# Optimization experiments

Measured on AMD Instinct MI355X. Metric: run time of the kernel, lower is better.

The kernel has to match this reference:

```python
import jax, jax.numpy as jnp
import numpy as np

B, LN, LT, D, DIN, H = 8, 64, 256, 1024, 2048, 4
LN_EPS = 1e-5
F16_EPS = float(np.finfo(np.float16).eps)


def setup_inputs() -> dict:
    key = jax.random.key(0)
    ks = jax.random.split(key, 16)
    n = lambda k, sh: jax.random.normal(k, sh, dtype=jnp.float32)
    s = 0.02
    z = lambda sh: jnp.zeros(sh, jnp.float32)
    return {
        "text_embeds": n(ks[0], (B, LT, D)),
        "node_embeds": n(ks[1], (B, LN, D)),
        "Wq": n(ks[2], (D, H * D)) * s, "bq": z((H * D,)),
        "Wk": n(ks[3], (D, H * D)) * s, "bk": z((H * D,)),
        "Wv": n(ks[4], (D, H * D)) * s, "bv": z((H * D,)),
        "Wo": n(ks[5], (H * D, D)) * s, "bo": z((D,)),
        "ln_g": jnp.ones((D,), jnp.float32), "ln_b": z((D,)),
        "aqW": n(ks[6], (D, D)) * s, "aqb": z((D,)),
        "akW": n(ks[7], (D, D)) * s, "akb": z((D,)),
        "att_v": n(ks[8], (D,)) * (1.0 / np.sqrt(D)),
        "att_b": z((D,)),
        "dp1W": n(ks[9], (D, DIN // 2)) * s, "dp1b": z((DIN // 2,)),
        "dp2W": n(ks[10], (DIN // 2, DIN)) * s, "dp2b": z((DIN,)),
        "gnn_mask": jax.random.randint(ks[11], (B, LN), 0, 2),
        "lm_mask": jax.random.randint(ks[12], (B, LT), 0, 2),
    }


def _forward(text_embeds, node_embeds, Wq, bq, Wk, bk, Wv, bv, Wo, bo, ln_g, ln_b,
             aqW, aqb, akW, akb, att_v, att_b, dp1W, dp1b, dp2W, dp2b,
             gnn_mask, lm_mask):
    x = node_embeds  # (B, LN, D)

    # ---- selfAttention_prompt: each of 4 heads has full width D ----
    def heads(w, b):
        return (x @ w + b).reshape(B, LN, H, D).transpose(0, 2, 1, 3)  # (B,H,LN,D)

    Q, K, V = heads(Wq, bq), heads(Wk, bk), heads(Wv, bv)
    A = jnp.einsum('bhqd,bhkd->bhqk', Q, K) / jnp.sqrt(jnp.float32(D))
    A = jnp.where(gnn_mask[:, None, None, :] == 0, -jnp.inf, A)
    alpha = jax.nn.softmax(A, axis=-1)
    out = jnp.einsum('bhqk,bhkd->bhqd', alpha, V)
    out = out.transpose(0, 2, 1, 3).reshape(B, LN, H * D)
    out = out @ Wo + bo + x
    # LayerNorm (torch default eps=1e-5)
    mu = out.mean(-1, keepdims=True)
    var = ((out - mu) ** 2).mean(-1, keepdims=True)
    H2 = (out - mu) / jnp.sqrt(var + LN_EPS) * ln_g + ln_b  # (B, LN, D)

    # ---- AdditiveAttention (Bahdanau): value_proj is unused in the original ----
    q = H2 @ aqW + aqb            # (B, LN, D)
    k = text_embeds @ akW + akb   # (B, LT, D)
    e = jnp.einsum('bqkd,d->bqk',
                   jnp.tanh(q[:, :, None, :] + k[:, None, :, :] + att_b), att_v)
    e = jnp.where(lm_mask[:, None, :] == 0, -jnp.inf, e)
    w = jax.nn.softmax(e, axis=-1)            # (B, LN, LT)
    H3 = jnp.einsum('bqk,bkd->bqd', w, text_embeds)  # context with raw V

    # ---- filter_Pool: masked mean over nodes ----
    m = gnn_mask.astype(H3.dtype)[:, :, None]
    cnt = jnp.clip(m.sum(1), F16_EPS, None)   # (B, 1)
    H4 = (H3 * m).sum(1) / cnt                # (B, D)

    # ---- domain projector (exact GELU like torch) ----
    Z = jax.nn.gelu(H4 @ dp1W + dp1b, approximate=False) @ dp2W + dp2b
    return Z  # (B, DIN)


def reference(text_embeds, node_embeds, Wq, bq, Wk, bk, Wv, bv, Wo, bo, ln_g, ln_b,
              aqW, aqb, akW, akb, att_v, att_b, dp1W, dp1b, dp2W, dp2b,
              gnn_mask, lm_mask):
    return _forward(text_embeds, node_embeds, Wq, bq, Wk, bk, Wv, bv, Wo, bo,
                    ln_g, ln_b, aqW, aqb, akW, akb, att_v, att_b,
                    dp1W, dp1b, dp2W, dp2b, gnn_mask, lm_mask)
```

## Files before the change

### kernel.cpp

```cpp
#include <hip/hip_runtime.h>
#include <hip/hip_bf16.h>
#include <math.h>

#define NB 8
#define LNN 64
#define LTN 256
#define DD 1024
#define NH 4
#define HDD 4096
#define DINN 2048
#define DHN 1024

#define C_TANH 2.8853900817779268f

typedef __bf16 bf16x8 __attribute__((ext_vector_type(8)));
typedef float f32x4 __attribute__((ext_vector_type(4)));

__device__ __forceinline__ float b2f(ushort u) {
  union { float f; unsigned int i; } x; x.i = ((unsigned int)u) << 16; return x.f;
}
__device__ __forceinline__ ushort f2b(float f) {
  unsigned int u = __builtin_bit_cast(unsigned int, f);
  u = (u + 0x7FFFu + ((u >> 16) & 1u)) >> 16;
  return (ushort)u;
}

__global__ __launch_bounds__(256) void cvt_all(const float* __restrict__ node,
                                               ushort* __restrict__ node_bf,
                                               const float* __restrict__ text,
                                               ushort* __restrict__ text_bf) {
  int bid = blockIdx.x;
  const float* in;
  ushort* out;
  int i;
  if (bid < 256) { in = node; out = node_bf; i = (bid * 256 + threadIdx.x) * 8; }
  else { in = text; out = text_bf; i = ((bid - 256) * 256 + threadIdx.x) * 8; }
  float4 a = *(const float4*)(in + i);
  float4 b = *(const float4*)(in + i + 4);
  ushort4 o0 = {f2b(a.x), f2b(a.y), f2b(a.z), f2b(a.w)};
  ushort4 o1 = {f2b(b.x), f2b(b.y), f2b(b.z), f2b(b.w)};
  *(ushort4*)(out + i) = o0;
  *(ushort4*)(out + i + 4) = o1;
}

__global__ __launch_bounds__(256) void tcvt3(const float* __restrict__ W0,
                                             const float* __restrict__ W1,
                                             const float* __restrict__ W2,
                                             ushort* __restrict__ Wt, int K, int N) {
  int z = blockIdx.z;
  const float* W = (z == 0) ? W0 : ((z == 1) ? W1 : W2);
  ushort* dst0 = Wt + (size_t)z * K * N;
  __shared__ float tf[64][65];
  int k0 = blockIdx.y << 6, n0 = blockIdx.x << 6;
  int t = threadIdx.x;
  int r = t >> 2, c4 = (t & 3) * 16;
  const float* src = W + (size_t)(k0 + r) * N + n0 + c4;
  float4 v0 = *(const float4*)(src);
  float4 v1 = *(const float4*)(src + 4);
  float4 v2 = *(const float4*)(src + 8);
  float4 v3 = *(const float4*)(src + 12);
  *(float4*)&tf[r][c4] = v0;
  *(float4*)&tf[r][c4 + 4] = v1;
  *(float4*)&tf[r][c4 + 8] = v2;
  *(float4*)&tf[r][c4 + 12] = v3;
  __syncthreads();
  int nl = t >> 2, kc = (t & 3) * 16;
  ushort tmp[16];
#pragma unroll
  for (int j = 0; j < 16; ++j) tmp[j] = f2b(tf[kc + j][nl]);
  ushort* dst = dst0 + (size_t)(n0 + nl) * K + k0 + kc;
  *(uint4*)(dst) = *(uint4*)&tmp[0];
  *(uint4*)(dst + 8) = *(uint4*)&tmp[8];
}

__global__ __launch_bounds__(256) void gemm_qkv3(const ushort* __restrict__ A,
                                                 const ushort* __restrict__ BtB,
                                                 const float* __restrict__ b0,
                                                 const float* __restrict__ b1,
                                                 const float* __restrict__ b2,
                                                 ushort* __restrict__ o0,
                                                 ushort* __restrict__ o1,
                                                 ushort* __restrict__ o2,
                                                 int M, int N, int K) {
  int z = blockIdx.z;
  const ushort* Bt = BtB + (size_t)z * N * K;
  const float* bias = (z == 0) ? b0 : ((z == 1) ? b1 : b2);
  ushort* Cout = (z == 0) ? o0 : ((z == 1) ? o1 : o2);
  __shared__ ushort Als[64 * 64];
  __shared__ ushort Bls[128 * 64];
  int tid = threadIdx.x;
  int m0 = blockIdx.y << 6, n0 = blockIdx.x << 7;
  int srow = tid >> 3, su = tid & 7;
  int sx = (su ^ (srow & 7)) * 8;
  const ushort* ga = A + (size_t)(m0 + srow) * K + su * 8;
  const ushort* gb = Bt + (size_t)(n0 + srow) * K + su * 8;
  int wa0 = srow * 64 + sx, wa1 = (srow + 32) * 64 + sx;
  int wb2 = (srow + 64) * 64 + sx, wb3 = (srow + 96) * 64 + sx;
  const size_t rs32 = (size_t)32 * K;
  int lane = tid & 63, w = tid >> 6;
  int wm = w >> 1, wn = w & 1;
  int r = lane & 15, kg = lane >> 4;
  f32x4 acc[2][4] = {};
  uint4 pa0 = *(const uint4*)(ga);
  uint4 pa1 = *(const uint4*)(ga + rs32);
  uint4 pb0 = *(const uint4*)(gb);
  uint4 pb1 = *(const uint4*)(gb + rs32);
  uint4 pb2 = *(const uint4*)(gb + 2 * rs32);
  uint4 pb3 = *(const uint4*)(gb + 3 * rs32);
  for (int k0 = 0; k0 < K; k0 += 64) {
    __syncthreads();
    *(uint4*)&Als[wa0] = pa0; *(uint4*)&Als[wa1] = pa1;
    *(uint4*)&Bls[wa0] = pb0; *(uint4*)&Bls[wa1] = pb1;
    *(uint4*)&Bls[wb2] = pb2; *(uint4*)&Bls[wb3] = pb3;
    __syncthreads();
    int kn = k0 + 64;
    if (kn < K) {
      pa0 = *(const uint4*)(ga + kn);
      pa1 = *(const uint4*)(ga + rs32 + kn);
      pb0 = *(const uint4*)(gb + kn);
      pb1 = *(const uint4*)(gb + rs32 + kn);
      pb2 = *(const uint4*)(gb + 2 * rs32 + kn);
      pb3 = *(const uint4*)(gb + 3 * rs32 + kn);
    }
#pragma unroll
    for (int h = 0; h < 2; ++h) {
      int sa = ((h * 4 + kg) ^ (r & 7)) * 8;
      bf16x8 af[2], bfr[4];
#pragma unroll
      for (int m = 0; m < 2; ++m)
        af[m] = *(const bf16x8*)&Als[(wm * 32 + m * 16 + r) * 64 + sa];
#pragma unroll
      for (int n = 0; n < 4; ++n)
        bfr[n] = *(const bf16x8*)&Bls[(wn * 64 + n * 16 + r) * 64 + sa];
#pragma unroll
      for (int m = 0; m < 2; ++m)
#pragma unroll
        for (int n = 0; n < 4; ++n)
          acc[m][n] = __builtin_amdgcn_mfma_f32_16x16x32_bf16(af[m], bfr[n], acc[m][n], 0, 0, 0);
    }
  }
#pragma unroll
  for (int m = 0; m < 2; ++m)
#pragma unroll
    for (int n = 0; n < 4; ++n) {
      f32x4 a = acc[m][n];
#pragma unroll
      for (int v = 0; v < 4; ++v) {
        int row = m0 + wm * 32 + m * 16 + kg * 4 + v;
        int col = n0 + wn * 64 + n * 16 + r;
        Cout[(size_t)row * N + col] = f2b(a[v] + bias[col]);
      }
    }
}

__global__ __launch_bounds__(256) void gemm_wo_split(const ushort* __restrict__ A,
                                                     const ushort* __restrict__ Bt,
                                                     float* __restrict__ P,
                                                     int M, int N, int K) {
  __shared__ ushort Als[64 * 64];
  __shared__ ushort Bls[128 * 64];
  int tid = threadIdx.x;
  int m0 = blockIdx.y << 6, n0 = blockIdx.x << 7;
  int Ks = K >> 2, kbase = blockIdx.z * Ks;
  int srow = tid >> 3, su = tid & 7;
  int sx = (su ^ (srow & 7)) * 8;
  const ushort* ga = A + (size_t)(m0 + srow) * K + kbase + su * 8;
  const ushort* gb = Bt + (size_t)(n0 + srow) * K + kbase + su * 8;
  int wa0 = srow * 64 + sx, wa1 = (srow + 32) * 64 + sx;
  int wb2 = (srow + 64) * 64 + sx, wb3 = (srow + 96) * 64 + sx;
  const size_t rs32 = (size_t)32 * K;
  int lane = tid & 63, w = tid >> 6;
  int wm = w >> 1, wn = w & 1;
  int r = lane & 15, kg = lane >> 4;
  f32x4 acc[2][4] = {};
  uint4 pa0 = *(const uint4*)(ga);
  uint4 pa1 = *(const uint4*)(ga + rs32);
  uint4 pb0 = *(const uint4*)(gb);
  uint4 pb1 = *(const uint4*)(gb + rs32);
  uint4 pb2 = *(const uint4*)(gb + 2 * rs32);
  uint4 pb3 = *(const uint4*)(gb + 3 * rs32);
  for (int k0 = 0; k0 < Ks; k0 += 64) {
    __syncthreads();
    *(uint4*)&Als[wa0] = pa0; *(uint4*)&Als[wa1] = pa1;
    *(uint4*)&Bls[wa0] = pb0; *(uint4*)&Bls[wa1] = pb1;
    *(uint4*)&Bls[wb2] = pb2; *(uint4*)&Bls[wb3] = pb3;
    __syncthreads();
    int kn = k0 + 64;
    if (kn < Ks) {
      pa0 = *(const uint4*)(ga + kn);
      pa1 = *(const uint4*)(ga + rs32 + kn);
      pb0 = *(const uint4*)(gb + kn);
      pb1 = *(const uint4*)(gb + rs32 + kn);
      pb2 = *(const uint4*)(gb + 2 * rs32 + kn);
      pb3 = *(const uint4*)(gb + 3 * rs32 + kn);
    }
#pragma unroll
    for (int h = 0; h < 2; ++h) {
      int sa = ((h * 4 + kg) ^ (r & 7)) * 8;
      bf16x8 af[2], bfr[4];
#pragma unroll
      for (int m = 0; m < 2; ++m)
        af[m] = *(const bf16x8*)&Als[(wm * 32 + m * 16 + r) * 64 + sa];
#pragma unroll
      for (int n = 0; n < 4; ++n)
        bfr[n] = *(const bf16x8*)&Bls[(wn * 64 + n * 16 + r) * 64 + sa];
#pragma unroll
      for (int m = 0; m < 2; ++m)
#pragma unroll
        for (int n = 0; n < 4; ++n)
          acc[m][n] = __builtin_amdgcn_mfma_f32_16x16x32_bf16(af[m], bfr[n], acc[m][n], 0, 0, 0);
    }
  }
#pragma unroll
  for (int m = 0; m < 2; ++m)
#pragma unroll
    for (int n = 0; n < 4; ++n) {
      f32x4 a = acc[m][n];
#pragma unroll
      for (int v = 0; v < 4; ++v) {
        int row = m0 + wm * 32 + m * 16 + kg * 4 + v;
        int col = n0 + wn * 64 + n * 16 + r;
        P[((size_t)blockIdx.z * M + row) * N + col] = a[v];
      }
    }
}

__global__ __launch_bounds__(256) void gemm_aqak(const ushort* __restrict__ H2,
                                                 const ushort* __restrict__ Tbf,
                                                 const ushort* __restrict__ TwtAQ,
                                                 const float* __restrict__ aqb,
                                                 const float* __restrict__ akb,
                                                 const float* __restrict__ attb,
                                                 float* __restrict__ QBu,
                                                 float* __restrict__ KAB,
                                                 int N, int K) {
  __shared__ ushort Als[64 * 64];
  __shared__ ushort Bls[128 * 64];
  int tid = threadIdx.x;
  int gm0 = blockIdx.y << 6, n0 = blockIdx.x << 7;
  const ushort* Abase;
  const ushort* Bt;
  const float* bias;
  const float* bias2;
  float* Obase;
  if (gm0 < 512) {
    Abase = H2 + (size_t)gm0 * K;
    Bt = TwtAQ;
    bias = aqb; bias2 = nullptr;
    Obase = QBu + (size_t)gm0 * N;
  } else {
    Abase = Tbf + (size_t)(gm0 - 512) * K;
    Bt = TwtAQ + (size_t)N * K;
    bias = akb; bias2 = attb;
    Obase = KAB + (size_t)(gm0 - 512) * N;
  }
  int srow = tid >> 3, su = tid & 7;
  int sx = (su ^ (srow & 7)) * 8;
  const ushort* ga = Abase + (size_t)srow * K + su * 8;
  const ushort* gb = Bt + (size_t)(n0 + srow) * K + su * 8;
  int wa0 = srow * 64 + sx, wa1 = (srow + 32) * 64 + sx;
  int wb2 = (srow + 64) * 64 + sx, wb3 = (srow + 96) * 64 + sx;
  const size_t rs32 = (size_t)32 * K;
  int lane = tid & 63, w = tid >> 6;
  int wm = w >> 1, wn = w & 1;
  int r = lane & 15, kg = lane >> 4;
  f32x4 acc[2][4] = {};
  uint4 pa0 = *(const uint4*)(ga);
  uint4 pa1 = *(const uint4*)(ga + rs32);
  uint4 pb0 = *(const uint4*)(gb);
  uint4 pb1 = *(const uint4*)(gb + rs32);
  uint4 pb2 = *(const uint4*)(gb + 2 * rs32);
  uint4 pb3 = *(const uint4*)(gb + 3 * rs32);
  for (int k0 = 0; k0 < K; k0 += 64) {
    __syncthreads();
    *(uint4*)&Als[wa0] = pa0; *(uint4*)&Als[wa1] = pa1;
    *(uint4*)&Bls[wa0] = pb0; *(uint4*)&Bls[wa1] = pb1;
    *(uint4*)&Bls[wb2] = pb2; *(uint4*)&Bls[wb3] = pb3;
    __syncthreads();
    int kn = k0 + 64;
    if (kn < K) {
      pa0 = *(const uint4*)(ga + kn);
      pa1 = *(const uint4*)(ga + rs32 + kn);
      pb0 = *(const uint4*)(gb + kn);
      pb1 = *(const uint4*)(gb + rs32 + kn);
      pb2 = *(const uint4*)(gb + 2 * rs32 + kn);
      pb3 = *(const uint4*)(gb + 3 * rs32 + kn);
    }
#pragma unroll
    for (int h = 0; h < 2; ++h) {
      int sa = ((h * 4 + kg) ^ (r & 7)) * 8;
      bf16x8 af[2], bfr[4];
#pragma unroll
      for (int m = 0; m < 2; ++m)
        af[m] = *(const bf16x8*)&Als[(wm * 32 + m * 16 + r) * 64 + sa];
#pragma unroll
      for (int n = 0; n < 4; ++n)
        bfr[n] = *(const bf16x8*)&Bls[(wn * 64 + n * 16 + r) * 64 + sa];
#pragma unroll
      for (int m = 0; m < 2; ++m)
#pragma unroll
        for (int n = 0; n < 4; ++n)
          acc[m][n] = __builtin_amdgcn_mfma_f32_16x16x32_bf16(af[m], bfr[n], acc[m][n], 0, 0, 0);
    }
  }
#pragma unroll
  for (int m = 0; m < 2; ++m)
#pragma unroll
    for (int n = 0; n < 4; ++n) {
      f32x4 a = acc[m][n];
#pragma unroll
      for (int v = 0; v < 4; ++v) {
        int lrow = wm * 32 + m * 16 + kg * 4 + v;
        int col = n0 + wn * 64 + n * 16 + r;
        float x = a[v] + bias[col];
        if (bias2) x += bias2[col];
        Obase[(size_t)lrow * N + col] = x * C_TANH;
      }
    }
}

__global__ __launch_bounds__(256) void wo_ln(const float* __restrict__ P,
                                             const float* __restrict__ bo,
                                             const float* __restrict__ node,
                                             const float* __restrict__ g,
                                             const float* __restrict__ be,
                                             ushort* __restrict__ Y) {
  int row = blockIdx.x, tid = threadIdx.x;
  int c = tid * 4;
  const size_t MN = (size_t)512 * 1024;
  size_t o = (size_t)row * DD + c;
  float4 v0 = *(const float4*)(P + o);
  float4 v1 = *(const float4*)(P + MN + o);
  float4 v2 = *(const float4*)(P + 2 * MN + o);
  float4 v3 = *(const float4*)(P + 3 * MN + o);
  float4 rv = *(const float4*)(node + o);
  float4 bv = *(const float4*)(bo + c);
  float4 v;
  v.x = v0.x + v1.x + v2.x + v3.x + rv.x + bv.x;
  v.y = v0.y + v1.y + v2.y + v3.y + rv.y + bv.y;
  v.z = v0.z + v1.z + v2.z + v3.z + rv.z + bv.z;
  v.w = v0.w + v1.w + v2.w + v3.w + rv.w + bv.w;
  float s = v.x + v.y + v.z + v.w;
  float ss = v.x * v.x + v.y * v.y + v.z * v.z + v.w * v.w;
  for (int o2 = 32; o2; o2 >>= 1) {
    s += __shfl_xor(s, o2, 64);
    ss += __shfl_xor(ss, o2, 64);
  }
  __shared__ float rb_[8];
  int lane = tid & 63, w = tid >> 6;
  if (lane == 0) { rb_[w] = s; rb_[4 + w] = ss; }
  __syncthreads();
  s = rb_[0] + rb_[1] + rb_[2] + rb_[3];
  ss = rb_[4] + rb_[5] + rb_[6] + rb_[7];
  float mu = s * (1.f / 1024.f);
  float var = ss * (1.f / 1024.f) - mu * mu;
  float rstd = rsqrtf(var + 1e-5f);
  ushort4 o4;
  o4.x = f2b((v.x - mu) * rstd * g[c + 0] + be[c + 0]);
  o4.y = f2b((v.y - mu) * rstd * g[c + 1] + be[c + 1]);
  o4.z = f2b((v.z - mu) * rstd * g[c + 2] + be[c + 2]);
  o4.w = f2b((v.w - mu) * rstd * g[c + 3] + be[c + 3]);
  *(ushort4*)(Y + (size_t)row * DD + c) = o4;
}

__global__ __launch_bounds__(256) void attn_fused(const ushort* __restrict__ Qb,
                                                  const ushort* __restrict__ Kb,
                                                  const ushort* __restrict__ Vb,
                                                  const int* __restrict__ gmask,
                                                  ushort* __restrict__ AO) {
  int bh = blockIdx.x;
  int b = bh >> 2;
  size_t base = ((size_t)b * LNN) * HDD + (size_t)(bh & 3) * DD;
  __shared__ ushort Als[64 * 64];
  __shared__ ushort Bls[64 * 64];
  __shared__ float S[64][68];
  __shared__ ushort Pls[64 * 72];
  __shared__ ushort Vt[64 * 72];
  int tid = threadIdx.x;
  int srow = tid >> 2, su0 = (tid & 3) * 2;
  const ushort* ga = Qb + base + (size_t)srow * HDD + su0 * 8;
  const ushort* gb = Kb + base + (size_t)srow * HDD + su0 * 8;
  int wa0 = srow * 64 + ((su0) ^ (srow & 7)) * 8;
  int wa1 = srow * 64 + ((su0 + 1) ^ (srow & 7)) * 8;
  int lane = tid & 63, w = tid >> 6;
  int wm = w >> 1, wn = w & 1;
  int r = lane & 15, kg = lane >> 4;
  {
    f32x4 acc[2][2] = {};
    uint4 pa0 = *(const uint4*)(ga);
    uint4 pa1 = *(const uint4*)(ga + 8);
    uint4 pb0 = *(const uint4*)(gb);
    uint4 pb1 = *(const uint4*)(gb + 8);
    for (int k0 = 0; k0 < DD; k0 += 64) {
      __syncthreads();
      *(uint4*)&Als[wa0] = pa0; *(uint4*)&Als[wa1] = pa1;
      *(uint4*)&Bls[wa0] = pb0; *(uint4*)&Bls[wa1] = pb1;
      __syncthreads();
      int kn = k0 + 64;
      if (kn < DD) {
        pa0 = *(const uint4*)(ga + kn);
        pa1 = *(const uint4*)(ga + kn + 8);
        pb0 = *(const uint4*)(gb + kn);
        pb1 = *(const uint4*)(gb + kn + 8);
      }
#pragma unroll
      for (int h = 0; h < 2; ++h) {
        int sa = ((h * 4 + kg) ^ (r & 7)) * 8;
        bf16x8 af[2], bfr[2];
#pragma unroll
        for (int m = 0; m < 2; ++m)
          af[m] = *(const bf16x8*)&Als[(wm * 32 + m * 16 + r) * 64 + sa];
#pragma unroll
        for (int n = 0; n < 2; ++n)
          bfr[n] = *(const bf16x8*)&Bls[(wn * 32 + n * 16 + r) * 64 + sa];
#pragma unroll
        for (int m = 0; m < 2; ++m)
#pragma unroll
          for (int n = 0; n < 2; ++n)
            acc[m][n] = __builtin_amdgcn_mfma_f32_16x16x32_bf16(af[m], bfr[n], acc[m][n], 0, 0, 0);
      }
    }
#pragma unroll
    for (int m = 0; m < 2; ++m)
#pragma unroll
      for (int n = 0; n < 2; ++n)
#pragma unroll
        for (int v = 0; v < 4; ++v)
          S[wm * 32 + m * 16 + kg * 4 + v][wn * 32 + n * 16 + r] = acc[m][n][v];
  }
  __syncthreads();
  bool valid = gmask[b * LNN + lane] != 0;
  for (int i = 0; i < 16; ++i) {
    int q = w * 16 + i;
    float v = valid ? S[q][lane] * 0.03125f : -__builtin_inff();
    float mx = v;
    for (int o = 32; o; o >>= 1) mx = fmaxf(mx, __shfl_xor(mx, o, 64));
    float e = valid ? __expf(v - mx) : 0.f;
    float s = e;
    for (int o = 32; o; o >>= 1) s += __shfl_xor(s, o, 64);
    Pls[q * 72 + lane] = f2b(__fdividef(e, s));
  }
  for (int dt = 0; dt < 16; ++dt) {
    int d0 = dt * 64;
    {
      int kq = tid >> 2, dq = (tid & 3) * 16;
      const ushort* src = Vb + base + (size_t)kq * HDD + d0 + dq;
      uint4 v0 = *(const uint4*)src;
      uint4 v1 = *(const uint4*)(src + 8);
      ushort tmp[16];
      *(uint4*)&tmp[0] = v0;
      *(uint4*)&tmp[8] = v1;
#pragma unroll
      for (int j = 0; j < 16; ++j) Vt[(dq + j) * 72 + kq] = tmp[j];
    }
    __syncthreads();
    f32x4 acc[2][2] = {};
#pragma unroll
    for (int h = 0; h < 2; ++h) {
      int ko = h * 32 + kg * 8;
      bf16x8 af[2], bfr[2];
#pragma unroll
      for (int m = 0; m < 2; ++m)
        af[m] = *(const bf16x8*)&Pls[(wm * 32 + m * 16 + r) * 72 + ko];
#pragma unroll
      for (int n = 0; n < 2; ++n)
        bfr[n] = *(const bf16x8*)&Vt[(wn * 32 + n * 16 + r) * 72 + ko];
#pragma unroll
      for (int m = 0; m < 2; ++m)
#pragma unroll
        for (int n = 0; n < 2; ++n)
          acc[m][n] = __builtin_amdgcn_mfma_f32_16x16x32_bf16(af[m], bfr[n], acc[m][n], 0, 0, 0);
    }
#pragma unroll
    for (int m = 0; m < 2; ++m)
#pragma unroll
      for (int n = 0; n < 2; ++n) {
        f32x4 a = acc[m][n];
#pragma unroll
        for (int v = 0; v < 4; ++v) {
          int q = wm * 32 + m * 16 + kg * 4 + v;
          int col = wn * 32 + n * 16 + r;
          AO[base + (size_t)q * HDD + d0 + col] = f2b(a[v]);
        }
      }
    __syncthreads();
  }
}

__global__ __launch_bounds__(256) void addatt_e(const float* __restrict__ QBu,
                                                const float* __restrict__ KAB,
                                                const float* __restrict__ av_,
                                                float* __restrict__ E4) {
  int dq = blockIdx.x, qt = blockIdx.y, b = blockIdx.z;
  int tid = threadIdx.x;
  __shared__ float qs[4][256];
  __shared__ float avs[256];
  __shared__ float red[4];
  int bq0 = b * LNN + qt * 4;
#pragma unroll
  for (int qq = 0; qq < 4; ++qq)
    qs[qq][tid] = QBu[(size_t)(bq0 + qq) * DD + dq * 256 + tid];
  float av = av_[dq * 256 + tid];
  avs[tid] = av;
  float s = av;
  for (int o = 32; o; o >>= 1) s += __shfl_xor(s, o, 64);
  int lane = tid & 63, w = tid >> 6;
  if (lane == 0) red[w] = s;
  __syncthreads();
  float sumav = red[0] + red[1] + red[2] + red[3];
  const float* kr = KAB + (size_t)(b * LTN + tid) * DD + dq * 256;
  float ac0 = 0.f, ac1 = 0.f, ac2 = 0.f, ac3 = 0.f;
#pragma unroll 2
  for (int d = 0; d < 256; d += 4) {
    float4 kv = *(const float4*)(kr + d);
    float4 av4 = *(const float4*)&avs[d];
    float4 q0 = *(const float4*)&qs[0][d];
    float4 q1 = *(const float4*)&qs[1][d];
    float4 q2 = *(const float4*)&qs[2][d];
    float4 q3 = *(const float4*)&qs[3][d];
    ac0 = fmaf(av4.x, __builtin_amdgcn_rcpf(__builtin_amdgcn_exp2f(q0.x + kv.x) + 1.f), ac0);
    ac1 = fmaf(av4.x, __builtin_amdgcn_rcpf(__builtin_amdgcn_exp2f(q1.x + kv.x) + 1.f), ac1);
    ac2 = fmaf(av4.x, __builtin_amdgcn_rcpf(__builtin_amdgcn_exp2f(q2.x + kv.x) + 1.f), ac2);
    ac3 = fmaf(av4.x, __builtin_amdgcn_rcpf(__builtin_amdgcn_exp2f(q3.x + kv.x) + 1.f), ac3);
    ac0 = fmaf(av4.y, __builtin_amdgcn_rcpf(__builtin_amdgcn_exp2f(q0.y + kv.y) + 1.f), ac0);
    ac1 = fmaf(av4.y, __builtin_amdgcn_rcpf(__builtin_amdgcn_exp2f(q1.y + kv.y) + 1.f), ac1);
    ac2 = fmaf(av4.y, __builtin_amdgcn_rcpf(__builtin_amdgcn_exp2f(q2.y + kv.y) + 1.f), ac2);
    ac3 = fmaf(av4.y, __builtin_amdgcn_rcpf(__builtin_amdgcn_exp2f(q3.y + kv.y) + 1.f), ac3);
    ac0 = fmaf(av4.z, __builtin_amdgcn_rcpf(__builtin_amdgcn_exp2f(q0.z + kv.z) + 1.f), ac0);
    ac1 = fmaf(av4.z, __builtin_amdgcn_rcpf(__builtin_amdgcn_exp2f(q1.z + kv.z) + 1.f), ac1);
    ac2 = fmaf(av4.z, __builtin_amdgcn_rcpf(__builtin_amdgcn_exp2f(q2.z + kv.z) + 1.f), ac2);
    ac3 = fmaf(av4.z, __builtin_amdgcn_rcpf(__builtin_amdgcn_exp2f(q3.z + kv.z) + 1.f), ac3);
    ac0 = fmaf(av4.w, __builtin_amdgcn_rcpf(__builtin_amdgcn_exp2f(q0.w + kv.w) + 1.f), ac0);
    ac1 = fmaf(av4.w, __builtin_amdgcn_rcpf(__builtin_amdgcn_exp2f(q1.w + kv.w) + 1.f), ac1);
    ac2 = fmaf(av4.w, __builtin_amdgcn_rcpf(__builtin_amdgcn_exp2f(q2.w + kv.w) + 1.f), ac2);
    ac3 = fmaf(av4.w, __builtin_amdgcn_rcpf(__builtin_amdgcn_exp2f(q3.w + kv.w) + 1.f), ac3);
  }
  size_t ebase = ((size_t)dq * 512 + bq0) * LTN + tid;
  E4[ebase] = sumav - 2.f * ac0;
  E4[ebase + LTN] = sumav - 2.f * ac1;
  E4[ebase + 2 * LTN] = sumav - 2.f * ac2;
  E4[ebase + 3 * LTN] = sumav - 2.f * ac3;
}

__global__ __launch_bounds__(256) void addatt_sm(const float* __restrict__ E4,
                                                 const int* __restrict__ lmask,
                                                 float* __restrict__ Wv) {
  int bq = blockIdx.x;
  int b = bq >> 6;
  int tid = threadIdx.x;
  __shared__ float rb_[8];
  float e = E4[(size_t)bq * LTN + tid] + E4[((size_t)512 + bq) * LTN + tid] +
            E4[((size_t)1024 + bq) * LTN + tid] + E4[((size_t)1536 + bq) * LTN + tid];
  bool valid = lmask[b * LTN + tid] != 0;
  float v = valid ? e : -__builtin_inff();
  int lane = tid & 63, w = tid >> 6;
  float m = v;
  for (int o = 32; o; o >>= 1) m = fmaxf(m, __shfl_xor(m, o, 64));
  if (lane == 0) rb_[w] = m;
  __syncthreads();
  m = fmaxf(fmaxf(rb_[0], rb_[1]), fmaxf(rb_[2], rb_[3]));
  float ex = valid ? __expf(v - m) : 0.f;
  float sm = ex;
  for (int o = 32; o; o >>= 1) sm += __shfl_xor(sm, o, 64);
  if (lane == 0) rb_[4 + w] = sm;
  __syncthreads();
  sm = rb_[4] + rb_[5] + rb_[6] + rb_[7];
  Wv[(size_t)bq * LTN + tid] = __fdividef(ex, sm);
}

__global__ __launch_bounds__(256) void addatt_pool(const float* __restrict__ Wv,
                                                   const float* __restrict__ text,
                                                   const int* __restrict__ gmask,
                                                   float* __restrict__ H4) {
  int dt = blockIdx.x, b = blockIdx.y;
  int tid = threadIdx.x;
  __shared__ float cf[LTN];
  float c = 0.f, cnt = 0.f;
#pragma unroll 8
  for (int q = 0; q < LNN; ++q) {
    float m = (gmask[b * LNN + q] != 0) ? 1.f : 0.f;
    cnt += m;
    c = fmaf(m, Wv[(size_t)(b * LNN + q) * LTN + tid], c);
  }
  cf[tid] = c;
  cnt = fmaxf(cnt, 9.765625e-04f);
  __syncthreads();
  int d = dt * 256 + tid;
  const float* tb = text + (size_t)b * LTN * DD + d;
  float acc = 0.f;
#pragma unroll 8
  for (int k = 0; k < LTN; ++k) acc = fmaf(cf[k], tb[(size_t)k * DD], acc);
  H4[b * DD + d] = acc / cnt;
}

__global__ __launch_bounds__(256) void dp_split(const float* __restrict__ X,
                                                const float* __restrict__ W,
                                                float* __restrict__ P,
                                                int K, int N) {
  int jt = blockIdx.x, kt = blockIdx.y;
  int t = threadIdx.x;
  __shared__ float xs[8][32];
  if (t < 64) {
    int b = t >> 3, kk = (t & 7) * 4;
    *(float4*)&xs[b][kk] = *(const float4*)(X + (size_t)b * K + kt * 32 + kk);
  }
  __syncthreads();
  int j = jt * 64 + (t & 63);
  int bg = (t >> 6) * 2;
  const float* wp = W + (size_t)(kt * 32) * N + j;
  float a0 = 0.f, a1 = 0.f;
#pragma unroll
  for (int k = 0; k < 32; ++k) {
    float w = wp[(size_t)k * N];
    a0 = fmaf(xs[bg + 0][k], w, a0);
    a1 = fmaf(xs[bg + 1][k], w, a1);
  }
  P[((size_t)kt * 8 + bg + 0) * N + j] = a0;
  P[((size_t)kt * 8 + bg + 1) * N + j] = a1;
}

template <int GELU>
__global__ __launch_bounds__(256) void dp_reduce(const float* __restrict__ P,
                                                 const float* __restrict__ bias,
                                                 float* __restrict__ O, int N) {
  int b = blockIdx.y;
  int j = blockIdx.x * 256 + threadIdx.x;
  float s = bias[j];
#pragma unroll 8
  for (int kt = 0; kt < 32; ++kt) s += P[((size_t)kt * 8 + b) * N + j];
  if constexpr (GELU) s = 0.5f * s * (1.f + erff(s * 0.70710678118654752440f));
  O[(size_t)b * N + j] = s;
}

extern "C" void kernel_launch(void* const* d_in, const int* in_sizes, int n_in,
                              void* d_out, int out_size, void* d_ws, size_t ws_size,
                              hipStream_t stream) {
  const float* text = (const float*)d_in[0];
  const float* node = (const float*)d_in[1];
  const float* Wq = (const float*)d_in[2];
  const float* bq = (const float*)d_in[3];
  const float* Wk = (const float*)d_in[4];
  const float* bk = (const float*)d_in[5];
  const float* Wv = (const float*)d_in[6];
  const float* bv = (const float*)d_in[7];
  const float* Wo = (const float*)d_in[8];
  const float* bo = (const float*)d_in[9];
  const float* lng = (const float*)d_in[10];
  const float* lnb = (const float*)d_in[11];
  const float* aqW = (const float*)d_in[12];
  const float* aqb = (const float*)d_in[13];
  const float* akW = (const float*)d_in[14];
  const float* akb = (const float*)d_in[15];
  const float* attv = (const float*)d_in[16];
  const float* attb = (const float*)d_in[17];
  const float* dp1W = (const float*)d_in[18];
  const float* dp1b = (const float*)d_in[19];
  const float* dp2W = (const float*)d_in[20];
  const float* dp2b = (const float*)d_in[21];
  const int* gmask = (const int*)d_in[22];
  const int* lmask = (const int*)d_in[23];
  (void)in_sizes; (void)n_in; (void)out_size;

  char* base = (char*)d_ws;
#define MB(x) (((size_t)(x)) << 20)
  ushort* Twt = (ushort*)(base);
  ushort* node_bf = (ushort*)(base + MB(8));
  ushort* text_bf = (ushort*)(base + MB(9));
  ushort* Qb = (ushort*)(base + MB(13));
  ushort* Kb = (ushort*)(base + MB(17));
  ushort* Vb = (ushort*)(base + MB(21));
  ushort* AO = (ushort*)(base + MB(25));
  float* E4 = (float*)(base + MB(13));
  float* Wvb = (float*)(base + MB(15));
  ushort* H2 = (ushort*)(base + MB(15) + (512 << 10));
  float* P_Wo = (float*)(base + MB(17));
  float* P1 = (float*)(base + MB(18));
  float* P2 = (float*)(base + MB(19));
  float* QBu = (float*)(base + MB(21));
  float* KAB = (float*)(base + MB(25));
  float* H4 = (float*)(base + MB(33));
  float* G = (float*)(base + MB(33) + 32768);
  ushort* TwtQKV = (ushort*)(base + MB(34));
  float* Z = (float*)d_out;
  const bool bigws = ws_size >= MB(59);
#undef MB

  const int M1 = NB * LNN;
  dim3 blk(256);

  cvt_all<<<dim3(1280), blk, 0, stream>>>(node, node_bf, text, text_bf);

  if (bigws) {
    tcvt3<<<dim3(HDD / 64, DD / 64, 3), blk, 0, stream>>>(Wq, Wk, Wv, TwtQKV, DD, HDD);
    gemm_qkv3<<<dim3(HDD / 128, M1 / 64, 3), blk, 0, stream>>>(node_bf, TwtQKV, bq, bk, bv, Qb, Kb, Vb, M1, HDD, DD);
  } else {
    tcvt3<<<dim3(HDD / 64, DD / 64, 1), blk, 0, stream>>>(Wq, Wq, Wq, Twt, DD, HDD);
    gemm_qkv3<<<dim3(HDD / 128, M1 / 64, 1), blk, 0, stream>>>(node_bf, Twt, bq, bq, bq, Qb, Qb, Qb, M1, HDD, DD);
    tcvt3<<<dim3(HDD / 64, DD / 64, 1), blk, 0, stream>>>(Wk, Wk, Wk, Twt, DD, HDD);
    gemm_qkv3<<<dim3(HDD / 128, M1 / 64, 1), blk, 0, stream>>>(node_bf, Twt, bk, bk, bk, Kb, Kb, Kb, M1, HDD, DD);
    tcvt3<<<dim3(HDD / 64, DD / 64, 1), blk, 0, stream>>>(Wv, Wv, Wv, Twt, DD, HDD);
    gemm_qkv3<<<dim3(HDD / 128, M1 / 64, 1), blk, 0, stream>>>(node_bf, Twt, bv, bv, bv, Vb, Vb, Vb, M1, HDD, DD);
  }

  attn_fused<<<dim3(NB * NH), blk, 0, stream>>>(Qb, Kb, Vb, gmask, AO);

  tcvt3<<<dim3(DD / 64, HDD / 64, 1), blk, 0, stream>>>(Wo, Wo, Wo, Twt, HDD, DD);
  gemm_wo_split<<<dim3(DD / 128, M1 / 64, 4), blk, 0, stream>>>(AO, Twt, P_Wo, M1, DD, HDD);
  wo_ln<<<dim3(M1), blk, 0, stream>>>(P_Wo, bo, node, lng, lnb, H2);

  tcvt3<<<dim3(DD / 64, DD / 64, 2), blk, 0, stream>>>(aqW, akW, akW, Twt, DD, DD);
  gemm_aqak<<<dim3(DD / 128, 40), blk, 0, stream>>>(H2, text_bf, Twt, aqb, akb, attb, QBu, KAB, DD, DD);

  addatt_e<<<dim3(4, 16, NB), blk, 0, stream>>>(QBu, KAB, attv, E4);
  addatt_sm<<<dim3(M1), blk, 0, stream>>>(E4, lmask, Wvb);
  addatt_pool<<<dim3(4, NB), blk, 0, stream>>>(Wvb, text, gmask, H4);

  dp_split<<<dim3(DHN / 64, 32), blk, 0, stream>>>(H4, dp1W, P1, DD, DHN);
  dp_reduce<1><<<dim3(DHN / 256, NB), blk, 0, stream>>>(P1, dp1b, G, DHN);
  dp_split<<<dim3(DINN / 64, 32), blk, 0, stream>>>(G, dp2W, P2, DHN, DINN);
  dp_reduce<0><<<dim3(DINN / 256, NB), blk, 0, stream>>>(P2, dp2b, Z, DINN);
}
```

Before: 184.3 us.

## Split fused attention into split-K QK kernel and tiled PV kernel

The single attention kernel ran only 32 blocks, each looping serially over the full 1024-wide head dimension for QK^T and then over 16 output tiles for PV. It is replaced by a split-K QK^T kernel (256 blocks writing fp32 partial scores to workspace) and a PV kernel (256 blocks) that sums the partials, recomputes softmax per block, and handles a 128-column output tile. The goal is to fill far more CUs on a severely underoccupied launch, at the cost of an extra launch, a workspace round trip for partial scores, and softmax being recomputed eight times per head.

Result: faster. 173.7 us (-5.8%).

```diff
diff --git a/kernel.cpp b/kernel.cpp
--- a/kernel.cpp
+++ b/kernel.cpp
@@ -363,19 +363,14 @@
   *(ushort4*)(Y + (size_t)row * DD + c) = o4;
 }
 
-__global__ __launch_bounds__(256) void attn_fused(const ushort* __restrict__ Qb,
-                                                  const ushort* __restrict__ Kb,
-                                                  const ushort* __restrict__ Vb,
-                                                  const int* __restrict__ gmask,
-                                                  ushort* __restrict__ AO) {
-  int bh = blockIdx.x;
+__global__ __launch_bounds__(256) void attn_qk(const ushort* __restrict__ Qb,
+                                               const ushort* __restrict__ Kb,
+                                               float* __restrict__ Sp) {
+  int bh = blockIdx.x, ks = blockIdx.y;
   int b = bh >> 2;
-  size_t base = ((size_t)b * LNN) * HDD + (size_t)(bh & 3) * DD;
+  size_t base = ((size_t)b * LNN) * HDD + (size_t)(bh & 3) * DD + ks * 128;
   __shared__ ushort Als[64 * 64];
   __shared__ ushort Bls[64 * 64];
-  __shared__ float S[64][68];
-  __shared__ ushort Pls[64 * 72];
-  __shared__ ushort Vt[64 * 72];
   int tid = threadIdx.x;
   int srow = tid >> 2, su0 = (tid & 3) * 2;
   const ushort* ga = Qb + base + (size_t)srow * HDD + su0 * 8;
@@ -385,48 +380,101 @@
   int lane = tid & 63, w = tid >> 6;
   int wm = w >> 1, wn = w & 1;
   int r = lane & 15, kg = lane >> 4;
+  f32x4 acc[2][2] = {};
+  uint4 pa0 = *(const uint4*)(ga);
+  uint4 pa1 = *(const uint4*)(ga + 8);
+  uint4 pb0 = *(const uint4*)(gb);
+  uint4 pb1 = *(const uint4*)(gb + 8);
+  for (int k0 = 0; k0 < 128; k0 += 64) {
+    __syncthreads();
+    *(uint4*)&Als[wa0] = pa0; *(uint4*)&Als[wa1] = pa1;
+    *(uint4*)&Bls[wa0] = pb0; *(uint4*)&Bls[wa1] = pb1;
+    __syncthreads();
+    if (k0 == 0) {
+      pa0 = *(const uint4*)(ga + 64);
+      pa1 = *(const uint4*)(ga + 64 + 8);
+      pb0 = *(const uint4*)(gb + 64);
+      pb1 = *(const uint4*)(gb + 64 + 8);
+    }
+#pragma unroll
+    for (int h = 0; h < 2; ++h) {
+      int sa = ((h * 4 + kg) ^ (r & 7)) * 8;
+      bf16x8 af[2], bfr[2];
+#pragma unroll
+      for (int m = 0; m < 2; ++m)
+        af[m] = *(const bf16x8*)&Als[(wm * 32 + m * 16 + r) * 64 + sa];
+#pragma unroll
+      for (int n = 0; n < 2; ++n)
+        bfr[n] = *(const bf16x8*)&Bls[(wn * 32 + n * 16 + r) * 64 + sa];
+#pragma unroll
+      for (int m = 0; m < 2; ++m)
+#pragma unroll
+        for (int n = 0; n < 2; ++n)
+          acc[m][n] = __builtin_amdgcn_mfma_f32_16x16x32_bf16(af[m], bfr[n], acc[m][n], 0, 0, 0);
+    }
+  }
+  float* out = Sp + ((size_t)ks * 32 + bh) * 4096;
+#pragma unroll
+  for (int m = 0; m < 2; ++m)
+#pragma unroll
+    for (int n = 0; n < 2; ++n) {
+      f32x4 a = acc[m][n];
+#pragma unroll
+      for (int v = 0; v < 4; ++v) {
+        int row = wm * 32 + m * 16 + kg * 4 + v;
+        int col = wn * 32 + n * 16 + r;
+        out[row * 64 + col] = a[v];
+      }
+    }
+}
+
+__global__ __launch_bounds__(256) void attn_pv(const float* __restrict__ Sp,
+                                               const ushort* __restrict__ Vb,
+                                               const int* __restrict__ gmask,
+                                               ushort* __restrict__ AO) {
+  int bid = blockIdx.x;
+  int bh = bid >> 3, dt = bid & 7;
+  int b = bh >> 2;
+  int d0 = dt * 128;
+  size_t base = ((size_t)b * LNN) * HDD + (size_t)(bh & 3) * DD;
+  __shared__ float S[64][68];
+  __shared__ ushort Pls[64 * 72];
+  __shared__ ushort Vt[128 * 72];
+  int tid = threadIdx.x;
+  int lane = tid & 63, w = tid >> 6;
   {
-    f32x4 acc[2][2] = {};
-    uint4 pa0 = *(const uint4*)(ga);
-    uint4 pa1 = *(const uint4*)(ga + 8);
-    uint4 pb0 = *(const uint4*)(gb);
-    uint4 pb1 = *(const uint4*)(gb + 8);
-    for (int k0 = 0; k0 < DD; k0 += 64) {
-      __syncthreads();
-      *(uint4*)&Als[wa0] = pa0; *(uint4*)&Als[wa1] = pa1;
-      *(uint4*)&Bls[wa0] = pb0; *(uint4*)&Bls[wa1] = pb1;
-      __syncthreads();
-      int kn = k0 + 64;
-      if (kn < DD) {
-        pa0 = *(const uint4*)(ga + kn);
-        pa1 = *(const uint4*)(ga + kn + 8);
-        pb0 = *(const uint4*)(gb + kn);
-        pb1 = *(const uint4*)(gb + kn + 8);
+    int fbase = tid * 16;
+    float a[16];
+#pragma unroll
+    for (int i = 0; i < 16; i += 4) {
+      float4 v = *(const float4*)(Sp + (size_t)bh * 4096 + fbase + i);
+      a[i] = v.x; a[i + 1] = v.y; a[i + 2] = v.z; a[i + 3] = v.w;
+    }
+#pragma unroll
+    for (int ks = 1; ks < 8; ++ks) {
+      const float* p = Sp + ((size_t)ks * 32 + bh) * 4096 + fbase;
+#pragma unroll
+      for (int i = 0; i < 16; i += 4) {
+        float4 v = *(const float4*)(p + i);
+        a[i] += v.x; a[i + 1] += v.y; a[i + 2] += v.z; a[i + 3] += v.w;
       }
-#pragma unroll
-      for (int h = 0; h < 2; ++h) {
-        int sa = ((h * 4 + kg) ^ (r & 7)) * 8;
-        bf16x8 af[2], bfr[2];
-#pragma unroll
-        for (int m = 0; m < 2; ++m)
-          af[m] = *(const bf16x8*)&Als[(wm * 32 + m * 16 + r) * 64 + sa];
-#pragma unroll
-        for (int n = 0; n < 2; ++n)
-          bfr[n] = *(const bf16x8*)&Bls[(wn * 32 + n * 16 + r) * 64 + sa];
-#pragma unroll
-        for (int m = 0; m < 2; ++m)
-#pragma unroll
-          for (int n = 0; n < 2; ++n)
-            acc[m][n] = __builtin_amdgcn_mfma_f32_16x16x32_bf16(af[m], bfr[n], acc[m][n], 0, 0, 0);
-      }
-    }
-#pragma unroll
-    for (int m = 0; m < 2; ++m)
-#pragma unroll
-      for (int n = 0; n < 2; ++n)
-#pragma unroll
-        for (int v = 0; v < 4; ++v)
-          S[wm * 32 + m * 16 + kg * 4 + v][wn * 32 + n * 16 + r] = acc[m][n][v];
+    }
+    int q = fbase >> 6, k = fbase & 63;
+#pragma unroll
+    for (int i = 0; i < 16; ++i) S[q][k + i] = a[i];
+  }
+  {
+    int kq = lane, dq = w * 32;
+    const ushort* src = Vb + base + (size_t)kq * HDD + d0 + dq;
+    uint4 v0 = *(const uint4*)src;
+    uint4 v1 = *(const uint4*)(src + 8);
+    uint4 v2 = *(const uint4*)(src + 16);
+    uint4 v3 = *(const uint4*)(src + 24);
+    ushort tmp[32];
+    *(uint4*)&tmp[0] = v0; *(uint4*)&tmp[8] = v1;
+    *(uint4*)&tmp[16] = v2; *(uint4*)&tmp[24] = v3;
+#pragma unroll
+    for (int j = 0; j < 32; ++j) Vt[(dq + j) * 72 + kq] = tmp[j];
   }
   __syncthreads();
   bool valid = gmask[b * LNN + lane] != 0;
@@ -440,51 +488,38 @@
     for (int o = 32; o; o >>= 1) s += __shfl_xor(s, o, 64);
     Pls[q * 72 + lane] = f2b(__fdividef(e, s));
   }
-  for (int dt = 0; dt < 16; ++dt) {
-    int d0 = dt * 64;
-    {
-      int kq = tid >> 2, dq = (tid & 3) * 16;
-      const ushort* src = Vb + base + (size_t)kq * HDD + d0 + dq;
-      uint4 v0 = *(const uint4*)src;
-      uint4 v1 = *(const uint4*)(src + 8);
-      ushort tmp[16];
-      *(uint4*)&tmp[0] = v0;
-      *(uint4*)&tmp[8] = v1;
-#pragma unroll
-      for (int j = 0; j < 16; ++j) Vt[(dq + j) * 72 + kq] = tmp[j];
-    }
-    __syncthreads();
-    f32x4 acc[2][2] = {};
-#pragma unroll
-    for (int h = 0; h < 2; ++h) {
-      int ko = h * 32 + kg * 8;
-      bf16x8 af[2], bfr[2];
-#pragma unroll
-      for (int m = 0; m < 2; ++m)
-        af[m] = *(const bf16x8*)&Pls[(wm * 32 + m * 16 + r) * 72 + ko];
-#pragma unroll
-      for (int n = 0; n < 2; ++n)
-        bfr[n] = *(const bf16x8*)&Vt[(wn * 32 + n * 16 + r) * 72 + ko];
-#pragma unroll
-      for (int m = 0; m < 2; ++m)
-#pragma unroll
-        for (int n = 0; n < 2; ++n)
-          acc[m][n] = __builtin_amdgcn_mfma_f32_16x16x32_bf16(af[m], bfr[n], acc[m][n], 0, 0, 0);
-    }
+  __syncthreads();
+  int wm = w >> 1, wn = w & 1;
+  int r = lane & 15, kg = lane >> 4;
+  f32x4 acc[2][4] = {};
+#pragma unroll
+  for (int h = 0; h < 2; ++h) {
+    int ko = h * 32 + kg * 8;
+    bf16x8 af[2], bfr[4];
 #pragma unroll
     for (int m = 0; m < 2; ++m)
-#pragma unroll
-      for (int n = 0; n < 2; ++n) {
-        f32x4 a = acc[m][n];
-#pragma unroll
-        for (int v = 0; v < 4; ++v) {
-          int q = wm * 32 + m * 16 + kg * 4 + v;
-          int col = wn * 32 + n * 16 + r;
-          AO[base + (size_t)q * HDD + d0 + col] = f2b(a[v]);
-        }
+      af[m] = *(const bf16x8*)&Pls[(wm * 32 + m * 16 + r) * 72 + ko];
+#pragma unroll
+    for (int n = 0; n < 4; ++n)
+      bfr[n] = *(const bf16x8*)&Vt[(wn * 64 + n * 16 + r) * 72 + ko];
+#pragma unroll
+    for (int m = 0; m < 2; ++m)
+#pragma unroll
+      for (int n = 0; n < 4; ++n)
+        acc[m][n] = __builtin_amdgcn_mfma_f32_16x16x32_bf16(af[m], bfr[n], acc[m][n], 0, 0, 0);
+  }
+#pragma unroll
+  for (int m = 0; m < 2; ++m)
+#pragma unroll
+    for (int n = 0; n < 4; ++n) {
+      f32x4 a = acc[m][n];
+#pragma unroll
+      for (int v = 0; v < 4; ++v) {
+        int q = wm * 32 + m * 16 + kg * 4 + v;
+        int col = wn * 64 + n * 16 + r;
+        AO[base + (size_t)q * HDD + d0 + col] = f2b(a[v]);
       }
-    __syncthreads();
-  }
+    }
 }
 
 __global__ __launch_bounds__(256) void addatt_e(const float* __restrict__ QBu,
@@ -664,6 +699,7 @@
   char* base = (char*)d_ws;
 #define MB(x) (((size_t)(x)) << 20)
   ushort* Twt = (ushort*)(base);
+  float* Sp = (float*)(base);
   ushort* node_bf = (ushort*)(base + MB(8));
   ushort* text_bf = (ushort*)(base + MB(9));
   ushort* Qb = (ushort*)(base + MB(13));
@@ -702,7 +738,8 @@
     gemm_qkv3<<<dim3(HDD / 128, M1 / 64, 1), blk, 0, stream>>>(node_bf, Twt, bv, bv, bv, Vb, Vb, Vb, M1, HDD, DD);
   }
 
-  attn_fused<<<dim3(NB * NH), blk, 0, stream>>>(Qb, Kb, Vb, gmask, AO);
+  attn_qk<<<dim3(NB * NH, 8), blk, 0, stream>>>(Qb, Kb, Sp);
+  attn_pv<<<dim3(NB * NH * 8), blk, 0, stream>>>(Sp, Vb, gmask, AO);
 
   tcvt3<<<dim3(DD / 64, HDD / 64, 1), blk, 0, stream>>>(Wo, Wo, Wo, Twt, HDD, DD);
   gemm_wo_split<<<dim3(DD / 128, M1 / 64, 4), blk, 0, stream>>>(AO, Twt, P_Wo, M1, DD, HDD);
```
